# Optimization experiments

Measured on AMD Instinct MI355X. Metric: run time of the kernel, lower is better.

The kernel has to match this reference:

```python
import jax, jax.numpy as jnp
import numpy as np

B, S, D = 8, 1024, 768
H = 12
DH = D // H  # 64


def setup_inputs() -> dict:
    key = jax.random.key(0)
    ks = jax.random.split(key, 9)
    s = 0.02
    return {
        "x": jax.random.normal(ks[0], (B, S, D), dtype=jnp.float32),
        # per-head QKV projections stacked over heads: [H, D, DH]
        "Wq": jax.random.normal(ks[1], (H, D, DH), dtype=jnp.float32) * s,
        "bq": jax.random.normal(ks[2], (H, DH), dtype=jnp.float32) * s,
        "Wk": jax.random.normal(ks[3], (H, D, DH), dtype=jnp.float32) * s,
        "bk": jax.random.normal(ks[4], (H, DH), dtype=jnp.float32) * s,
        "Wv": jax.random.normal(ks[5], (H, D, DH), dtype=jnp.float32) * s,
        "bv": jax.random.normal(ks[6], (H, DH), dtype=jnp.float32) * s,
        # output projection: [D, D] (applied as x @ Wo + bo)
        "Wo": jax.random.normal(ks[7], (D, D), dtype=jnp.float32) * s,
        "bo": jax.random.normal(ks[8], (D,), dtype=jnp.float32) * s,
    }


def reference(x, Wq, bq, Wk, bk, Wv, bv, Wo, bo):
    # Per-head linear projections, vectorized over heads -> [B, H, S, DH]
    q = jnp.einsum("bsd,hde->bhse", x, Wq) + bq[None, :, None, :]
    k = jnp.einsum("bsd,hde->bhse", x, Wk) + bk[None, :, None, :]
    v = jnp.einsum("bsd,hde->bhse", x, Wv) + bv[None, :, None, :]
    scale = 1.0 / jnp.sqrt(jnp.asarray(DH, dtype=q.dtype))
    scores = jnp.einsum("bhse,bhte->bhst", q, k) * scale  # [B,H,S,S]
    probs = jax.nn.softmax(scores, axis=-1)  # dropout p=0 (eval)
    out = jnp.einsum("bhst,bhte->bhse", probs, v)  # [B,H,S,DH]
    # concat heads (head order matches ModuleList order) -> [B,S,D]
    out = out.transpose(0, 2, 1, 3).reshape(B, S, D)
    return out @ Wo + bo
```

## Files before the change

kernel.cpp:

```cpp
#include <hip/hip_runtime.h>
#include <math.h>

#define BB 8
#define SS 1024
#define DD 768
#define HH 12
#define DHH 64
#define BSS (BB*SS)
#define NQKV 2304

typedef _Float16 half8 __attribute__((ext_vector_type(8)));
typedef _Float16 half4 __attribute__((ext_vector_type(4)));
typedef float    f32x4 __attribute__((ext_vector_type(4)));

__device__ __forceinline__
void transpose_tile(const float* __restrict__ src, _Float16* __restrict__ dst,
                    int d0, int n_outer, int base_mul, int row_stride, int tid)
{
    __shared__ float T[64][65];
    const size_t base = (size_t)n_outer * base_mul;
    {
        int dl = tid >> 2, c0 = (tid & 3) * 16;
        const float* p = src + base + (size_t)(d0 + dl) * row_stride + c0;
#pragma unroll
        for (int m = 0; m < 4; ++m) {
            float4 f = *(const float4*)(p + m * 4);
            T[dl][c0 + m*4 + 0] = f.x;
            T[dl][c0 + m*4 + 1] = f.y;
            T[dl][c0 + m*4 + 2] = f.z;
            T[dl][c0 + m*4 + 3] = f.w;
        }
    }
    __syncthreads();
    {
        int e = tid >> 2, c = tid & 3;
        half8 lo, hi;
#pragma unroll
        for (int i = 0; i < 8; ++i) {
            lo[i] = (_Float16)T[c*16 + i][e];
            hi[i] = (_Float16)T[c*16 + 8 + i][e];
        }
        _Float16* q = dst + ((size_t)n_outer * 64 + e) * DD + d0 + c * 16;
        *(half8*)q = lo;
        *(half8*)(q + 8) = hi;
    }
}

__global__ __launch_bounds__(256)
void transpose_all(const float* __restrict__ Wq, const float* __restrict__ Wk,
                   const float* __restrict__ Wv, const float* __restrict__ Wo,
                   _Float16* __restrict__ Wt, _Float16* __restrict__ Wot)
{
    const int z = blockIdx.z;
    const float* src;
    _Float16* dst;
    int base_mul, row_stride;
    if (z < 3) {
        src = (z == 0) ? Wq : (z == 1) ? Wk : Wv;
        dst = Wt + (size_t)z * DD * DD;
        base_mul = DD * DHH; row_stride = DHH;
    } else {
        src = Wo; dst = Wot;
        base_mul = 64; row_stride = DD;
    }
    transpose_tile(src, dst, blockIdx.x * 64, blockIdx.y, base_mul, row_stride,
                   threadIdx.x);
}

__global__ __launch_bounds__(256)
void gemm_qkv_stacked(const float* __restrict__ X, const _Float16* __restrict__ Wt,
                      const float* __restrict__ bq, const float* __restrict__ bk,
                      const float* __restrict__ bv,
                      _Float16* __restrict__ qo, _Float16* __restrict__ ko,
                      _Float16* __restrict__ vto)
{
    __shared__ _Float16 Ash[128][40];
    __shared__ _Float16 Bsh[128][40];

    const int b = blockIdx.x;
    const int c  = b & 7;
    const int g  = b >> 3;
    const int n_t = g % 18;
    const int m_t = (g / 18) * 8 + c;
    const int m0 = m_t * 128;
    const int n0 = n_t * 128;

    const int tid  = threadIdx.x;
    const int wave = tid >> 6;
    const int lane = tid & 15;
    const int quad = (tid >> 4) & 3;
    const int wy = wave >> 1;
    const int wx = wave & 1;

    f32x4 acc[4][4];
#pragma unroll
    for (int i = 0; i < 4; ++i)
#pragma unroll
        for (int j = 0; j < 4; ++j) acc[i][j] = (f32x4){0.f, 0.f, 0.f, 0.f};

    const int st_row = 0;
    (void)st_row;

    for (int k0 = 0; k0 < DD; k0 += 32) {
        __syncthreads();
#pragma unroll
        for (int cc = 0; cc < 2; ++cc) {
            int chunk = tid + cc * 256;
            int row = chunk >> 2, col8 = chunk & 3;
            const float* src = X + (size_t)(m0 + row) * DD + k0 + col8 * 8;
            float4 u = *(const float4*)src;
            float4 u2 = *(const float4*)(src + 4);
            half8 hv = { (_Float16)u.x, (_Float16)u.y, (_Float16)u.z, (_Float16)u.w,
                         (_Float16)u2.x, (_Float16)u2.y, (_Float16)u2.z, (_Float16)u2.w };
            *(half8*)&Ash[row][col8 * 8] = hv;
        }
#pragma unroll
        for (int cc = 0; cc < 2; ++cc) {
            int chunk = tid + cc * 256;
            int row = chunk >> 2, col8 = chunk & 3;
            *(half8*)&Bsh[row][col8 * 8] =
                *(const half8*)(Wt + (size_t)(n0 + row) * DD + k0 + col8 * 8);
        }
        __syncthreads();

        half8 a[4], bf[4];
#pragma unroll
        for (int i = 0; i < 4; ++i)
            a[i] = *(const half8*)&Ash[wy * 64 + i * 16 + lane][quad * 8];
#pragma unroll
        for (int j = 0; j < 4; ++j)
            bf[j] = *(const half8*)&Bsh[wx * 64 + j * 16 + lane][quad * 8];
#pragma unroll
        for (int i = 0; i < 4; ++i)
#pragma unroll
            for (int j = 0; j < 4; ++j)
                acc[i][j] = __builtin_amdgcn_mfma_f32_16x16x32_f16(a[i], bf[j], acc[i][j], 0, 0, 0);
    }

    const int w = n0 / 768;
    const float* bp = (w == 0) ? bq : (w == 1) ? bk : bv;
    const int nb = n0 - w * 768 + wx * 64;

#pragma unroll
    for (int i = 0; i < 4; ++i) {
#pragma unroll
        for (int r = 0; r < 4; ++r) {
            int row = m0 + wy * 64 + i * 16 + quad * 4 + r;
            int b_ = row >> 10;
            int s  = row & (SS - 1);
#pragma unroll
            for (int j = 0; j < 4; ++j) {
                int nl = nb + j * 16 + lane;
                int h = nl >> 6, e = nl & 63;
                float val = acc[i][j][r] + bp[nl];
                if (w == 0)
                    qo[((size_t)(b_ * HH + h) * SS + s) * DHH + e] = (_Float16)val;
                else if (w == 1)
                    ko[((size_t)(b_ * HH + h) * SS + s) * DHH + e] = (_Float16)val;
                else
                    vto[((size_t)(b_ * HH + h) * DHH + e) * SS + s] = (_Float16)val;
            }
        }
    }
}

__global__ __launch_bounds__(256)
void gemm_out_f16(const _Float16* __restrict__ Ah, const _Float16* __restrict__ Bt,
                  const float* __restrict__ bias, float* __restrict__ out)
{
    __shared__ _Float16 Ash[128][40];
    __shared__ _Float16 Bsh[64][40];
    const int tid  = threadIdx.x;
    const int wave = tid >> 6;
    const int lane = tid & 15;
    const int quad = (tid >> 4) & 3;
    const int m0 = blockIdx.x * 128;
    const int n0 = blockIdx.y * 64;

    f32x4 acc[2][4];
#pragma unroll
    for (int i = 0; i < 2; ++i)
#pragma unroll
        for (int j = 0; j < 4; ++j) acc[i][j] = (f32x4){0.f, 0.f, 0.f, 0.f};

    for (int k0 = 0; k0 < DD; k0 += 32) {
        __syncthreads();
#pragma unroll
        for (int cc = 0; cc < 2; ++cc) {
            int chunk = tid + cc * 256;
            int r = chunk >> 2, hf = chunk & 3;
            *(half8*)&Ash[r][hf * 8] =
                *(const half8*)(Ah + (size_t)(m0 + r) * DD + k0 + hf * 8);
        }
        {
            int r = tid >> 2, hf = tid & 3;
            *(half8*)&Bsh[r][hf * 8] =
                *(const half8*)(Bt + (size_t)(n0 + r) * DD + k0 + hf * 8);
        }
        __syncthreads();

        half8 a[2], bfr[4];
#pragma unroll
        for (int i = 0; i < 2; ++i)
            a[i] = *(const half8*)&Ash[wave * 32 + i * 16 + lane][quad * 8];
#pragma unroll
        for (int j = 0; j < 4; ++j)
            bfr[j] = *(const half8*)&Bsh[j * 16 + lane][quad * 8];
#pragma unroll
        for (int i = 0; i < 2; ++i)
#pragma unroll
            for (int j = 0; j < 4; ++j)
                acc[i][j] = __builtin_amdgcn_mfma_f32_16x16x32_f16(a[i], bfr[j], acc[i][j], 0, 0, 0);
    }

#pragma unroll
    for (int i = 0; i < 2; ++i) {
#pragma unroll
        for (int r = 0; r < 4; ++r) {
            int row = m0 + wave * 32 + i * 16 + quad * 4 + r;
#pragma unroll
            for (int j = 0; j < 4; ++j) {
                int col = n0 + j * 16 + lane;
                out[(size_t)row * DD + col] = acc[i][j][r] + bias[col];
            }
        }
    }
}

__global__ __launch_bounds__(256)
void attn_f16(const _Float16* __restrict__ qh, const _Float16* __restrict__ kh,
              const _Float16* __restrict__ vt, _Float16* __restrict__ ctxh)
{
    const int bh  = blockIdx.x;
    const int q0  = blockIdx.y * 64;
    const int tid = threadIdx.x;
    const int wave = tid >> 6;
    const int lane = tid & 15;
    const int quad = (tid >> 4) & 3;

    __shared__ _Float16 Qs[64][72];
    __shared__ _Float16 Ks[64][72];
    __shared__ _Float16 Vt[64][72];
    __shared__ _Float16 Pt[4][16][72];

    const _Float16* qb  = qh + ((size_t)bh * SS + q0) * DHH;
    const _Float16* kb  = kh + (size_t)bh * SS * DHH;
    const _Float16* vtb = vt + (size_t)bh * DHH * SS;

    {
        int r = tid >> 2, c0 = (tid & 3) * 16;
        half8 q1 = *(const half8*)(qb + (size_t)r * DHH + c0);
        half8 q2 = *(const half8*)(qb + (size_t)r * DHH + c0 + 8);
        q1 = q1 * (_Float16)0.125f;
        q2 = q2 * (_Float16)0.125f;
        *(half8*)&Qs[r][c0]     = q1;
        *(half8*)&Qs[r][c0 + 8] = q2;
    }
    __syncthreads();

    const half8 qlo = *(const half8*)&Qs[wave * 16 + lane][quad * 8];
    const half8 qhi = *(const half8*)&Qs[wave * 16 + lane][32 + quad * 8];

    f32x4 o[4];
    float lacc = 0.f;
#pragma unroll
    for (int j = 0; j < 4; ++j) o[j] = (f32x4){0.f, 0.f, 0.f, 0.f};

    for (int kt = 0; kt < SS; kt += 64) {
        __syncthreads();
        {
            int r = tid >> 2, c0 = (tid & 3) * 16;
            *(half8*)&Ks[r][c0]     = *(const half8*)(kb + (size_t)(kt + r) * DHH + c0);
            *(half8*)&Ks[r][c0 + 8] = *(const half8*)(kb + (size_t)(kt + r) * DHH + c0 + 8);
            *(half8*)&Vt[r][c0]     = *(const half8*)(vtb + (size_t)r * SS + kt + c0);
            *(half8*)&Vt[r][c0 + 8] = *(const half8*)(vtb + (size_t)r * SS + kt + c0 + 8);
        }
        __syncthreads();

#pragma unroll
        for (int f = 0; f < 4; ++f) {
            half8 klo = *(const half8*)&Ks[f * 16 + lane][quad * 8];
            half8 khi = *(const half8*)&Ks[f * 16 + lane][32 + quad * 8];
            f32x4 z = (f32x4){0.f, 0.f, 0.f, 0.f};
            z = __builtin_amdgcn_mfma_f32_16x16x32_f16(klo, qlo, z, 0, 0, 0);
            z = __builtin_amdgcn_mfma_f32_16x16x32_f16(khi, qhi, z, 0, 0, 0);
            half4 pk;
#pragma unroll
            for (int r = 0; r < 4; ++r) {
                float p = __expf(z[r]);
                lacc += p;
                pk[r] = (_Float16)p;
            }
            *(half4*)&Pt[wave][lane][f * 16 + quad * 4] = pk;
        }

        half8 pl = *(const half8*)&Pt[wave][lane][quad * 8];
        half8 ph = *(const half8*)&Pt[wave][lane][32 + quad * 8];

#pragma unroll
        for (int j = 0; j < 4; ++j) {
            half8 vlo = *(const half8*)&Vt[j * 16 + lane][quad * 8];
            half8 vhi = *(const half8*)&Vt[j * 16 + lane][32 + quad * 8];
            o[j] = __builtin_amdgcn_mfma_f32_16x16x32_f16(pl, vlo, o[j], 0, 0, 0);
            o[j] = __builtin_amdgcn_mfma_f32_16x16x32_f16(ph, vhi, o[j], 0, 0, 0);
        }
    }

    float lr = lacc;
    lr += __shfl_xor(lr, 16);
    lr += __shfl_xor(lr, 32);

    const int b_ = bh / HH;
    const int h_ = bh % HH;
#pragma unroll
    for (int r = 0; r < 4; ++r) {
        float invl = 1.f / __shfl(lr, quad * 4 + r, 16);
        int s_ = q0 + wave * 16 + quad * 4 + r;
        _Float16* orow = ctxh + ((size_t)(b_ * SS + s_)) * DD + h_ * DHH;
#pragma unroll
        for (int j = 0; j < 4; ++j)
            orow[j * 16 + lane] = (_Float16)(o[j][r] * invl);
    }
}

extern "C" void kernel_launch(void* const* d_in, const int* in_sizes, int n_in,
                              void* d_out, int out_size, void* d_ws, size_t ws_size,
                              hipStream_t stream)
{
    const float* x  = (const float*)d_in[0];
    const float* Wq = (const float*)d_in[1];
    const float* bq = (const float*)d_in[2];
    const float* Wk = (const float*)d_in[3];
    const float* bk = (const float*)d_in[4];
    const float* Wv = (const float*)d_in[5];
    const float* bv = (const float*)d_in[6];
    const float* Wo = (const float*)d_in[7];
    const float* bo = (const float*)d_in[8];
    float* out = (float*)d_out;

    const size_t xe = (size_t)BSS * DD;
    const size_t we = (size_t)DD * DD;
    _Float16* Wt   = (_Float16*)d_ws;
    _Float16* Wot  = Wt  + (size_t)3 * we;
    _Float16* qhb  = Wot + we;
    _Float16* khb  = qhb + xe;
    _Float16* vtb  = khb + xe;
    _Float16* ctxh = vtb + xe;

    dim3 tg(DD / 64, DD / 64, 4);
    transpose_all<<<tg, 256, 0, stream>>>(Wq, Wk, Wv, Wo, Wt, Wot);

    gemm_qkv_stacked<<<(BSS / 128) * (NQKV / 128), 256, 0, stream>>>(
        x, Wt, bq, bk, bv, qhb, khb, vtb);

    dim3 ag(BB * HH, SS / 64);
    attn_f16<<<ag, 256, 0, stream>>>(qhb, khb, vtb, ctxh);

    dim3 gg(BSS / 128, DD / 64);
    gemm_out_f16<<<gg, 256, 0, stream>>>(ctxh, Wot, bo, out);
}
```

Baseline: 237.1 us.

## Use direct global-to-LDS loads, pre-cast X to fp16, fold Q scale, enlarge out-GEMM tile

```diff
diff --git a/kernel.cpp b/kernel.cpp
--- a/kernel.cpp
+++ b/kernel.cpp
@@ -12,6 +12,25 @@
 typedef _Float16 half8 __attribute__((ext_vector_type(8)));
 typedef _Float16 half4 __attribute__((ext_vector_type(4)));
 typedef float    f32x4 __attribute__((ext_vector_type(4)));
+
+__device__ __forceinline__ void glds16(const _Float16* g, _Float16* l)
+{
+    __builtin_amdgcn_global_load_lds(
+        (const __attribute__((address_space(1))) uint32_t*)(g),
+        (__attribute__((address_space(3))) uint32_t*)(l),
+        16, 0, 0);
+}
+
+__global__ __launch_bounds__(256)
+void cast_x_f16(const float* __restrict__ x, _Float16* __restrict__ xh)
+{
+    int i = blockIdx.x * 256 + threadIdx.x;
+    const float4* xp = (const float4*)x + (size_t)i * 2;
+    float4 u = xp[0], v = xp[1];
+    half8 h = { (_Float16)u.x, (_Float16)u.y, (_Float16)u.z, (_Float16)u.w,
+                (_Float16)v.x, (_Float16)v.y, (_Float16)v.z, (_Float16)v.w };
+    ((half8*)xh)[i] = h;
+}
 
 __device__ __forceinline__
 void transpose_tile(const float* __restrict__ src, _Float16* __restrict__ dst,
@@ -68,14 +87,14 @@
 }
 
 __global__ __launch_bounds__(256)
-void gemm_qkv_stacked(const float* __restrict__ X, const _Float16* __restrict__ Wt,
+void gemm_qkv_stacked(const _Float16* __restrict__ Xh, const _Float16* __restrict__ Wt,
                       const float* __restrict__ bq, const float* __restrict__ bk,
                       const float* __restrict__ bv,
                       _Float16* __restrict__ qo, _Float16* __restrict__ ko,
                       _Float16* __restrict__ vto)
 {
-    __shared__ _Float16 Ash[128][40];
-    __shared__ _Float16 Bsh[128][40];
+    __shared__ _Float16 Ash[128][32];
+    __shared__ _Float16 Bsh[128][32];
 
     const int b = blockIdx.x;
     const int c  = b & 7;
@@ -87,49 +106,41 @@
 
     const int tid  = threadIdx.x;
     const int wave = tid >> 6;
-    const int lane = tid & 15;
+    const int lane = tid & 63;
+    const int l16  = tid & 15;
     const int quad = (tid >> 4) & 3;
     const int wy = wave >> 1;
     const int wx = wave & 1;
 
+    const _Float16* ap = Xh + (size_t)(m0 + 32 * wave + (lane >> 2)) * DD + (lane & 3) * 8;
+    const _Float16* bp = Wt + (size_t)(n0 + 32 * wave + (lane >> 2)) * DD + (lane & 3) * 8;
+    _Float16* ldsA0 = &Ash[32 * wave][0];
+    _Float16* ldsA1 = &Ash[32 * wave + 16][0];
+    _Float16* ldsB0 = &Bsh[32 * wave][0];
+    _Float16* ldsB1 = &Bsh[32 * wave + 16][0];
+
     f32x4 acc[4][4];
 #pragma unroll
     for (int i = 0; i < 4; ++i)
 #pragma unroll
         for (int j = 0; j < 4; ++j) acc[i][j] = (f32x4){0.f, 0.f, 0.f, 0.f};
 
-    const int st_row = 0;
-    (void)st_row;
-
     for (int k0 = 0; k0 < DD; k0 += 32) {
         __syncthreads();
-#pragma unroll
-        for (int cc = 0; cc < 2; ++cc) {
-            int chunk = tid + cc * 256;
-            int row = chunk >> 2, col8 = chunk & 3;
-            const float* src = X + (size_t)(m0 + row) * DD + k0 + col8 * 8;
-            float4 u = *(const float4*)src;
-            float4 u2 = *(const float4*)(src + 4);
-            half8 hv = { (_Float16)u.x, (_Float16)u.y, (_Float16)u.z, (_Float16)u.w,
-                         (_Float16)u2.x, (_Float16)u2.y, (_Float16)u2.z, (_Float16)u2.w };
-            *(half8*)&Ash[row][col8 * 8] = hv;
-        }
-#pragma unroll
-        for (int cc = 0; cc < 2; ++cc) {
-            int chunk = tid + cc * 256;
-            int row = chunk >> 2, col8 = chunk & 3;
-            *(half8*)&Bsh[row][col8 * 8] =
-                *(const half8*)(Wt + (size_t)(n0 + row) * DD + k0 + col8 * 8);
-        }
+        glds16(ap, ldsA0);
+        glds16(ap + 16 * DD, ldsA1);
+        glds16(bp, ldsB0);
+        glds16(bp + 16 * DD, ldsB1);
+        ap += 32; bp += 32;
         __syncthreads();
 
         half8 a[4], bf[4];
 #pragma unroll
         for (int i = 0; i < 4; ++i)
-            a[i] = *(const half8*)&Ash[wy * 64 + i * 16 + lane][quad * 8];
+            a[i] = *(const half8*)&Ash[wy * 64 + i * 16 + l16][quad * 8];
 #pragma unroll
         for (int j = 0; j < 4; ++j)
-            bf[j] = *(const half8*)&Bsh[wx * 64 + j * 16 + lane][quad * 8];
+            bf[j] = *(const half8*)&Bsh[wx * 64 + j * 16 + l16][quad * 8];
 #pragma unroll
         for (int i = 0; i < 4; ++i)
 #pragma unroll
@@ -138,8 +149,9 @@
     }
 
     const int w = n0 / 768;
-    const float* bp = (w == 0) ? bq : (w == 1) ? bk : bv;
+    const float* bp_ = (w == 0) ? bq : (w == 1) ? bk : bv;
     const int nb = n0 - w * 768 + wx * 64;
+    const float qscale = (w == 0) ? 0.125f : 1.0f;
 
 #pragma unroll
     for (int i = 0; i < 4; ++i) {
@@ -150,9 +162,9 @@
             int s  = row & (SS - 1);
 #pragma unroll
             for (int j = 0; j < 4; ++j) {
-                int nl = nb + j * 16 + lane;
+                int nl = nb + j * 16 + l16;
                 int h = nl >> 6, e = nl & 63;
-                float val = acc[i][j][r] + bp[nl];
+                float val = (acc[i][j][r] + bp_[nl]) * qscale;
                 if (w == 0)
                     qo[((size_t)(b_ * HH + h) * SS + s) * DHH + e] = (_Float16)val;
                 else if (w == 1)
@@ -168,59 +180,63 @@
 void gemm_out_f16(const _Float16* __restrict__ Ah, const _Float16* __restrict__ Bt,
                   const float* __restrict__ bias, float* __restrict__ out)
 {
-    __shared__ _Float16 Ash[128][40];
-    __shared__ _Float16 Bsh[64][40];
+    __shared__ _Float16 Ash[128][32];
+    __shared__ _Float16 Bsh[128][32];
+
+    const int m0 = blockIdx.x * 128;
+    const int n0 = blockIdx.y * 128;
     const int tid  = threadIdx.x;
     const int wave = tid >> 6;
-    const int lane = tid & 15;
+    const int lane = tid & 63;
+    const int l16  = tid & 15;
     const int quad = (tid >> 4) & 3;
-    const int m0 = blockIdx.x * 128;
-    const int n0 = blockIdx.y * 64;
-
-    f32x4 acc[2][4];
-#pragma unroll
-    for (int i = 0; i < 2; ++i)
+    const int wy = wave >> 1;
+    const int wx = wave & 1;
+
+    const _Float16* ap = Ah + (size_t)(m0 + 32 * wave + (lane >> 2)) * DD + (lane & 3) * 8;
+    const _Float16* bp = Bt + (size_t)(n0 + 32 * wave + (lane >> 2)) * DD + (lane & 3) * 8;
+    _Float16* ldsA0 = &Ash[32 * wave][0];
+    _Float16* ldsA1 = &Ash[32 * wave + 16][0];
+    _Float16* ldsB0 = &Bsh[32 * wave][0];
+    _Float16* ldsB1 = &Bsh[32 * wave + 16][0];
+
+    f32x4 acc[4][4];
+#pragma unroll
+    for (int i = 0; i < 4; ++i)
 #pragma unroll
         for (int j = 0; j < 4; ++j) acc[i][j] = (f32x4){0.f, 0.f, 0.f, 0.f};
 
     for (int k0 = 0; k0 < DD; k0 += 32) {
         __syncthreads();
-#pragma unroll
-        for (int cc = 0; cc < 2; ++cc) {
-            int chunk = tid + cc * 256;
-            int r = chunk >> 2, hf = chunk & 3;
-            *(half8*)&Ash[r][hf * 8] =
-                *(const half8*)(Ah + (size_t)(m0 + r) * DD + k0 + hf * 8);
-        }
-        {
-            int r = tid >> 2, hf = tid & 3;
-            *(half8*)&Bsh[r][hf * 8] =
-                *(const half8*)(Bt + (size_t)(n0 + r) * DD + k0 + hf * 8);
-        }
-        __syncthreads();
-
-        half8 a[2], bfr[4];
-#pragma unroll
-        for (int i = 0; i < 2; ++i)
-            a[i] = *(const half8*)&Ash[wave * 32 + i * 16 + lane][quad * 8];
+        glds16(ap, ldsA0);
+        glds16(ap + 16 * DD, ldsA1);
+        glds16(bp, ldsB0);
+        glds16(bp + 16 * DD, ldsB1);
+        ap += 32; bp += 32;
+        __syncthreads();
+
+        half8 a[4], bf[4];
+#pragma unroll
+        for (int i = 0; i < 4; ++i)
+            a[i] = *(const half8*)&Ash[wy * 64 + i * 16 + l16][quad * 8];
 #pragma unroll
         for (int j = 0; j < 4; ++j)
-            bfr[j] = *(const half8*)&Bsh[j * 16 + lane][quad * 8];
-#pragma unroll
-        for (int i = 0; i < 2; ++i)
+            bf[j] = *(const half8*)&Bsh[wx * 64 + j * 16 + l16][quad * 8];
+#pragma unroll
+        for (int i = 0; i < 4; ++i)
 #pragma unroll
             for (int j = 0; j < 4; ++j)
-                acc[i][j] = __builtin_amdgcn_mfma_f32_16x16x32_f16(a[i], bfr[j], acc[i][j], 0, 0, 0);
-    }
-
-#pragma unroll
-    for (int i = 0; i < 2; ++i) {
+                acc[i][j] = __builtin_amdgcn_mfma_f32_16x16x32_f16(a[i], bf[j], acc[i][j], 0, 0, 0);
+    }
+
+#pragma unroll
+    for (int i = 0; i < 4; ++i) {
 #pragma unroll
         for (int r = 0; r < 4; ++r) {
-            int row = m0 + wave * 32 + i * 16 + quad * 4 + r;
+            int row = m0 + wy * 64 + i * 16 + quad * 4 + r;
 #pragma unroll
             for (int j = 0; j < 4; ++j) {
-                int col = n0 + j * 16 + lane;
+                int col = n0 + wx * 64 + j * 16 + l16;
                 out[(size_t)row * DD + col] = acc[i][j][r] + bias[col];
             }
         }
@@ -235,31 +251,31 @@
     const int q0  = blockIdx.y * 64;
     const int tid = threadIdx.x;
     const int wave = tid >> 6;
-    const int lane = tid & 15;
+    const int lane = tid & 63;
+    const int l16  = tid & 15;
     const int quad = (tid >> 4) & 3;
 
-    __shared__ _Float16 Qs[64][72];
-    __shared__ _Float16 Ks[64][72];
-    __shared__ _Float16 Vt[64][72];
+    __shared__ _Float16 Qs[64][64];
+    __shared__ _Float16 Ks[64][64];
+    __shared__ _Float16 Vt[64][64];
     __shared__ _Float16 Pt[4][16][72];
 
     const _Float16* qb  = qh + ((size_t)bh * SS + q0) * DHH;
     const _Float16* kb  = kh + (size_t)bh * SS * DHH;
     const _Float16* vtb = vt + (size_t)bh * DHH * SS;
 
-    {
-        int r = tid >> 2, c0 = (tid & 3) * 16;
-        half8 q1 = *(const half8*)(qb + (size_t)r * DHH + c0);
-        half8 q2 = *(const half8*)(qb + (size_t)r * DHH + c0 + 8);
-        q1 = q1 * (_Float16)0.125f;
-        q2 = q2 * (_Float16)0.125f;
-        *(half8*)&Qs[r][c0]     = q1;
-        *(half8*)&Qs[r][c0 + 8] = q2;
-    }
+    const int srow = 16 * wave + (lane >> 3);
+    const int scol = (lane & 7) * 8;
+    const _Float16* qp = qb + (size_t)srow * DHH + scol;
+    const _Float16* kp = kb + (size_t)srow * DHH + scol;
+    const _Float16* vp = vtb + (size_t)srow * SS + scol;
+
+    glds16(qp, &Qs[16 * wave][0]);
+    glds16(qp + 8 * DHH, &Qs[16 * wave + 8][0]);
     __syncthreads();
 
-    const half8 qlo = *(const half8*)&Qs[wave * 16 + lane][quad * 8];
-    const half8 qhi = *(const half8*)&Qs[wave * 16 + lane][32 + quad * 8];
+    const half8 qlo = *(const half8*)&Qs[wave * 16 + l16][quad * 8];
+    const half8 qhi = *(const half8*)&Qs[wave * 16 + l16][32 + quad * 8];
 
     f32x4 o[4];
     float lacc = 0.f;
@@ -268,19 +284,18 @@
 
     for (int kt = 0; kt < SS; kt += 64) {
         __syncthreads();
-        {
-            int r = tid >> 2, c0 = (tid & 3) * 16;
-            *(half8*)&Ks[r][c0]     = *(const half8*)(kb + (size_t)(kt + r) * DHH + c0);
-            *(half8*)&Ks[r][c0 + 8] = *(const half8*)(kb + (size_t)(kt + r) * DHH + c0 + 8);
-            *(half8*)&Vt[r][c0]     = *(const half8*)(vtb + (size_t)r * SS + kt + c0);
-            *(half8*)&Vt[r][c0 + 8] = *(const half8*)(vtb + (size_t)r * SS + kt + c0 + 8);
-        }
+        glds16(kp, &Ks[16 * wave][0]);
+        glds16(kp + 8 * DHH, &Ks[16 * wave + 8][0]);
+        glds16(vp, &Vt[16 * wave][0]);
+        glds16(vp + 8 * SS, &Vt[16 * wave + 8][0]);
+        kp += 64 * DHH;
+        vp += 64;
         __syncthreads();
 
 #pragma unroll
         for (int f = 0; f < 4; ++f) {
-            half8 klo = *(const half8*)&Ks[f * 16 + lane][quad * 8];
-            half8 khi = *(const half8*)&Ks[f * 16 + lane][32 + quad * 8];
+            half8 klo = *(const half8*)&Ks[f * 16 + l16][quad * 8];
+            half8 khi = *(const half8*)&Ks[f * 16 + l16][32 + quad * 8];
             f32x4 z = (f32x4){0.f, 0.f, 0.f, 0.f};
             z = __builtin_amdgcn_mfma_f32_16x16x32_f16(klo, qlo, z, 0, 0, 0);
             z = __builtin_amdgcn_mfma_f32_16x16x32_f16(khi, qhi, z, 0, 0, 0);
@@ -291,16 +306,16 @@
                 lacc += p;
                 pk[r] = (_Float16)p;
             }
-            *(half4*)&Pt[wave][lane][f * 16 + quad * 4] = pk;
-        }
-
-        half8 pl = *(const half8*)&Pt[wave][lane][quad * 8];
-        half8 ph = *(const half8*)&Pt[wave][lane][32 + quad * 8];
+            *(half4*)&Pt[wave][l16][f * 16 + quad * 4] = pk;
+        }
+
+        half8 pl = *(const half8*)&Pt[wave][l16][quad * 8];
+        half8 ph = *(const half8*)&Pt[wave][l16][32 + quad * 8];
 
 #pragma unroll
         for (int j = 0; j < 4; ++j) {
-            half8 vlo = *(const half8*)&Vt[j * 16 + lane][quad * 8];
-            half8 vhi = *(const half8*)&Vt[j * 16 + lane][32 + quad * 8];
+            half8 vlo = *(const half8*)&Vt[j * 16 + l16][quad * 8];
+            half8 vhi = *(const half8*)&Vt[j * 16 + l16][32 + quad * 8];
             o[j] = __builtin_amdgcn_mfma_f32_16x16x32_f16(pl, vlo, o[j], 0, 0, 0);
             o[j] = __builtin_amdgcn_mfma_f32_16x16x32_f16(ph, vhi, o[j], 0, 0, 0);
         }
@@ -319,7 +334,7 @@
         _Float16* orow = ctxh + ((size_t)(b_ * SS + s_)) * DD + h_ * DHH;
 #pragma unroll
         for (int j = 0; j < 4; ++j)
-            orow[j * 16 + lane] = (_Float16)(o[j][r] * invl);
+            orow[j * 16 + l16] = (_Float16)(o[j][r] * invl);
     }
 }
 
@@ -340,22 +355,25 @@
 
     const size_t xe = (size_t)BSS * DD;
     const size_t we = (size_t)DD * DD;
-    _Float16* Wt   = (_Float16*)d_ws;
+    _Float16* Xh   = (_Float16*)d_ws;
+    _Float16* Wt   = Xh  + xe;
     _Float16* Wot  = Wt  + (size_t)3 * we;
     _Float16* qhb  = Wot + we;
     _Float16* khb  = qhb + xe;
     _Float16* vtb  = khb + xe;
     _Float16* ctxh = vtb + xe;
 
+    cast_x_f16<<<xe / 8 / 256, 256, 0, stream>>>(x, Xh);
+
     dim3 tg(DD / 64, DD / 64, 4);
     transpose_all<<<tg, 256, 0, stream>>>(Wq, Wk, Wv, Wo, Wt, Wot);
 
     gemm_qkv_stacked<<<(BSS / 128) * (NQKV / 128), 256, 0, stream>>>(
-        x, Wt, bq, bk, bv, qhb, khb, vtb);
+        Xh, Wt, bq, bk, bv, qhb, khb, vtb);
 
     dim3 ag(BB * HH, SS / 64);
     attn_f16<<<ag, 256, 0, stream>>>(qhb, khb, vtb, ctxh);
 
-    dim3 gg(BSS / 128, DD / 64);
+    dim3 gg(BSS / 128, DD / 128);
     gemm_out_f16<<<gg, 256, 0, stream>>>(ctxh, Wot, bo, out);
 }
```

Result: no change. 240.1 us (+1.3%).
